# Kernel tuning notes

Hardware: AMD Instinct MI355X
Metric: run time of the kernel (lower is better)

## Reference

```python
import jax, jax.numpy as jnp
import numpy as np

E, P, T, B = 512, 128, 1024, 1


def _lstm_dir(x, wih, whh, bih, bhh, reverse):
    # x: [B, T, Din]; torch LSTM gate order: i, f, g, o
    Bb = x.shape[0]
    H = whh.shape[1]
    xg = jnp.einsum('btd,gd->btg', x, wih) + bih + bhh  # [B, T, 4H]
    xg = jnp.swapaxes(xg, 0, 1)  # [T, B, 4H]

    def step(carry, g_t):
        h, c = carry
        g = g_t + h @ whh.T
        i, f, gg, o = jnp.split(g, 4, axis=-1)
        c = jax.nn.sigmoid(f) * c + jax.nn.sigmoid(i) * jnp.tanh(gg)
        h = jax.nn.sigmoid(o) * jnp.tanh(c)
        return (h, c), h

    h0 = jnp.zeros((Bb, H), x.dtype)
    _, hs = jax.lax.scan(step, (h0, h0), xg, reverse=reverse)
    return jnp.swapaxes(hs, 0, 1)  # [B, T, H]


def _bilstm(x, layers):
    for wih, whh, bih, bhh in layers:
        f = _lstm_dir(x, wih[0], whh[0], bih[0], bhh[0], False)
        b = _lstm_dir(x, wih[1], whh[1], bih[1], bhh[1], True)
        x = jnp.concatenate([f, b], axis=-1)
    return x


def setup_inputs() -> dict:
    key = jax.random.key(0)
    ks = jax.random.split(key, 20)
    s = 0.05
    d = {
        'words': jax.random.normal(ks[0], (B, T, E), jnp.float32),
        'pos': jax.random.normal(ks[1], (B, T, P), jnp.float32),
        'w_w0_ih': s * jax.random.normal(ks[2], (2, 4 * E, E), jnp.float32),
        'w_w0_hh': s * jax.random.normal(ks[3], (2, 4 * E, E), jnp.float32),
        'w_b0_ih': s * jax.random.normal(ks[4], (2, 4 * E), jnp.float32),
        'w_b0_hh': s * jax.random.normal(ks[5], (2, 4 * E), jnp.float32),
        'w_w1_ih': s * jax.random.normal(ks[6], (2, 4 * E, 2 * E), jnp.float32),
        'w_w1_hh': s * jax.random.normal(ks[7], (2, 4 * E, E), jnp.float32),
        'w_b1_ih': s * jax.random.normal(ks[8], (2, 4 * E), jnp.float32),
        'w_b1_hh': s * jax.random.normal(ks[9], (2, 4 * E), jnp.float32),
        'p_w0_ih': s * jax.random.normal(ks[10], (2, 4 * P, P), jnp.float32),
        'p_w0_hh': s * jax.random.normal(ks[11], (2, 4 * P, P), jnp.float32),
        'p_b0_ih': s * jax.random.normal(ks[12], (2, 4 * P), jnp.float32),
        'p_b0_hh': s * jax.random.normal(ks[13], (2, 4 * P), jnp.float32),
        'p_w1_ih': s * jax.random.normal(ks[14], (2, 4 * P, 2 * P), jnp.float32),
        'p_w1_hh': s * jax.random.normal(ks[15], (2, 4 * P, P), jnp.float32),
        'p_b1_ih': s * jax.random.normal(ks[16], (2, 4 * P), jnp.float32),
        'p_b1_hh': s * jax.random.normal(ks[17], (2, 4 * P), jnp.float32),
        'edge_w': s * jax.random.normal(ks[18], (1, 4 * (E + P)), jnp.float32),
        'edge_b': s * jax.random.normal(ks[19], (1,), jnp.float32),
    }
    return d


def reference(words, pos, w_w0_ih, w_w0_hh, w_b0_ih, w_b0_hh, w_w1_ih, w_w1_hh,
              w_b1_ih, w_b1_hh, p_w0_ih, p_w0_hh, p_b0_ih, p_b0_hh, p_w1_ih,
              p_w1_hh, p_b1_ih, p_b1_hh, edge_w, edge_b):
    hw = _bilstm(words, [(w_w0_ih, w_w0_hh, w_b0_ih, w_b0_hh),
                         (w_w1_ih, w_w1_hh, w_b1_ih, w_b1_hh)])  # [B,T,2E]
    hp = _bilstm(pos, [(p_w0_ih, p_w0_hh, p_b0_ih, p_b0_hh),
                       (p_w1_ih, p_w1_hh, p_b1_ih, p_b1_hh)])    # [B,T,2P]
    H = jnp.concatenate([hw, hp], axis=-1)[0]  # [T, 2(E+P)]
    D = H.shape[-1]
    # edge_scorer(concat(h_i, h_j)) = h_i @ W1 + h_j @ W2 + b
    s1 = H @ edge_w[0, :D]  # [T]
    s2 = H @ edge_w[0, D:]  # [T]
    S = s1[:, None] + s2[None, :] + edge_b[0]
    n = H.shape[0]
    eye = jnp.eye(n, dtype=bool)
    return jnp.where(eye, jnp.zeros((), S.dtype), S)  # diagonal stays 0
```

## Files before the change

### kernel.cpp

```cpp
#include <hip/hip_runtime.h>


#define T_LEN 1024

__global__ void poison_kernel(unsigned* p, int n) {
  int i = blockIdx.x * blockDim.x + threadIdx.x;
  int stride = gridDim.x * blockDim.x;
  for (; i < n; i += stride) p[i] = 0xFFFFFFFFu;
}

__global__ __launch_bounds__(256) void gemm_bt(
    const float* __restrict__ A,
    const float* __restrict__ Wt,
    const float* __restrict__ B0,
    const float* __restrict__ B1,
    float* __restrict__ C,
    int M, int N, int K)
{
  const int z = blockIdx.z;
  const float* W  = Wt + (size_t)z * N * K;
  const float* b0 = B0 + (size_t)z * N;
  const float* b1 = B1 + (size_t)z * N;
  float* Cz = C + (size_t)z * M * N;

  __shared__ __align__(16) float As[16][64];
  __shared__ __align__(16) float Ws[16][64];

  const int tid = threadIdx.x;
  const int tx = tid & 15, ty = tid >> 4;
  const int brow = blockIdx.y * 64, bcol = blockIdx.x * 64;
  const int lr = tid >> 2;
  const int lk = (tid & 3) << 2;

  float acc[4][4] = {};

  for (int k0 = 0; k0 < K; k0 += 16) {
    float4 av = *(const float4*)(A + (size_t)(brow + lr) * K + k0 + lk);
    float4 wv = *(const float4*)(W + (size_t)(bcol + lr) * K + k0 + lk);
    __syncthreads();
    As[lk + 0][lr] = av.x; As[lk + 1][lr] = av.y;
    As[lk + 2][lr] = av.z; As[lk + 3][lr] = av.w;
    Ws[lk + 0][lr] = wv.x; Ws[lk + 1][lr] = wv.y;
    Ws[lk + 2][lr] = wv.z; Ws[lk + 3][lr] = wv.w;
    __syncthreads();
    #pragma unroll
    for (int kk = 0; kk < 16; ++kk) {
      float4 a = *(const float4*)&As[kk][ty << 2];
      float4 w = *(const float4*)&Ws[kk][tx << 2];
      float a4[4] = {a.x, a.y, a.z, a.w};
      float w4[4] = {w.x, w.y, w.z, w.w};
      #pragma unroll
      for (int i = 0; i < 4; ++i)
        #pragma unroll
        for (int j = 0; j < 4; ++j)
          acc[i][j] = fmaf(a4[i], w4[j], acc[i][j]);
    }
  }

  const int nb = bcol + (tx << 2);
  float bias[4];
  #pragma unroll
  for (int j = 0; j < 4; ++j) bias[j] = b0[nb + j] + b1[nb + j];
  #pragma unroll
  for (int i = 0; i < 4; ++i) {
    int m = brow + (ty << 2) + i;
    float4 out;
    out.x = acc[i][0] + bias[0];
    out.y = acc[i][1] + bias[1];
    out.z = acc[i][2] + bias[2];
    out.w = acc[i][3] + bias[3];
    *(float4*)(Cz + (size_t)m * N + nb) = out;
  }
}

__device__ __forceinline__ float fsigmoid(float x) {
  return 1.f / (1.f + __expf(-x));
}
__device__ __forceinline__ float ftanh(float x) {
  return 2.f / (1.f + __expf(-2.f * x)) - 1.f;
}

template<int CTRL>
__device__ __forceinline__ float dpp_add(float v) {
  int x = __builtin_amdgcn_update_dpp(0, __float_as_int(v), CTRL, 0xf, 0xf, true);
  return v + __int_as_float(x);
}

__device__ __forceinline__ void word_body(
    int wg, const float* __restrict__ xg, const float* __restrict__ whh,
    float* hbuf, int rev)
{
  const int tid  = threadIdx.x;
  const int wave = tid >> 6;
  const int lane = tid & 63;
  const int p    = lane & 31;
  const int half = lane >> 5;
  const int eloc = wave * 2 + half;
  const int e    = wg * 16 + eloc;

  float4 wv[4][4];
  #pragma unroll
  for (int g = 0; g < 4; ++g) {
    const float* row = whh + (size_t)(g * 512 + e) * 512 + 4 * p;
    #pragma unroll
    for (int k = 0; k < 4; ++k)
      wv[g][k] = *(const float4*)(row + 128 * k);
  }

  __shared__ __align__(16) float h_lds[512];
  __shared__ __align__(16) float4 hgates[16];

  unsigned* hb = (unsigned*)hbuf;
  unsigned long long* hb64 = (unsigned long long*)hbuf;

  const bool tail = (tid < 16);
  float cst = 0.f;
  float xg4[4] = {0.f, 0.f, 0.f, 0.f};
  if (tail) {
    const int t0 = rev ? (T_LEN - 1) : 0;
    #pragma unroll
    for (int g = 0; g < 4; ++g)
      xg4[g] = xg[(size_t)t0 * 2048 + g * 512 + wg * 16 + tid];
  }

  for (int s = 0; s < T_LEN; ++s) {
    const int t = rev ? (T_LEN - 1 - s) : s;

    if (tid < 256) {
      float2 v;
      if (s == 0) {
        v.x = 0.f; v.y = 0.f;
      } else {
        const int tp = rev ? (t + 1) : (t - 1);
        unsigned long long u = __hip_atomic_load(hb64 + (size_t)tp * 256 + tid,
                                                 __ATOMIC_RELAXED,
                                                 __HIP_MEMORY_SCOPE_AGENT);
        while ((unsigned)u == 0xFFFFFFFFu || (unsigned)(u >> 32) == 0xFFFFFFFFu)
          u = __hip_atomic_load(hb64 + (size_t)tp * 256 + tid,
                                __ATOMIC_RELAXED, __HIP_MEMORY_SCOPE_AGENT);
        v.x = __uint_as_float((unsigned)u);
        v.y = __uint_as_float((unsigned)(u >> 32));
      }
      *(float2*)&h_lds[2 * tid] = v;
    }
    __syncthreads();

    float a0 = 0.f, a1 = 0.f, a2 = 0.f, a3 = 0.f;
    #pragma unroll
    for (int k = 0; k < 4; ++k) {
      float4 hv = *(const float4*)&h_lds[128 * k + 4 * p];
      float h4[4] = {hv.x, hv.y, hv.z, hv.w};
      #pragma unroll
      for (int j = 0; j < 4; ++j) {
        a0 = fmaf(wv[0][k].x * 0.f + ((const float*)&wv[0][k])[j], h4[j], a0);
        a1 = fmaf(((const float*)&wv[1][k])[j], h4[j], a1);
        a2 = fmaf(((const float*)&wv[2][k])[j], h4[j], a2);
        a3 = fmaf(((const float*)&wv[3][k])[j], h4[j], a3);
      }
    }

    a0 = dpp_add<0xB1>(a0);  a1 = dpp_add<0xB1>(a1);
    a2 = dpp_add<0xB1>(a2);  a3 = dpp_add<0xB1>(a3);
    a0 = dpp_add<0x4E>(a0);  a1 = dpp_add<0x4E>(a1);
    a2 = dpp_add<0x4E>(a2);  a3 = dpp_add<0x4E>(a3);
    a0 = dpp_add<0x141>(a0); a1 = dpp_add<0x141>(a1);
    a2 = dpp_add<0x141>(a2); a3 = dpp_add<0x141>(a3);
    a0 = dpp_add<0x140>(a0); a1 = dpp_add<0x140>(a1);
    a2 = dpp_add<0x140>(a2); a3 = dpp_add<0x140>(a3);
    a0 = dpp_add<0x142>(a0); a1 = dpp_add<0x142>(a1);
    a2 = dpp_add<0x142>(a2); a3 = dpp_add<0x142>(a3);

    if (p == 16) {
      float4 gsum; gsum.x = a0; gsum.y = a1; gsum.z = a2; gsum.w = a3;
      hgates[eloc] = gsum;
    }
    __syncthreads();

    if (tail) {
      float4 g4 = hgates[tid];
      float si = fsigmoid(g4.x + xg4[0]);
      float sf = fsigmoid(g4.y + xg4[1]);
      float tg = ftanh  (g4.z + xg4[2]);
      float so = fsigmoid(g4.w + xg4[3]);
      cst = fmaf(sf, cst, si * tg);
      float h = so * ftanh(cst);
      __hip_atomic_store(hb + (size_t)t * 512 + wg * 16 + tid,
                         __float_as_uint(h),
                         __ATOMIC_RELAXED, __HIP_MEMORY_SCOPE_AGENT);
      if (s + 1 < T_LEN) {
        const int tn = rev ? (t - 1) : (t + 1);
        #pragma unroll
        for (int g = 0; g < 4; ++g)
          xg4[g] = xg[(size_t)tn * 2048 + g * 512 + wg * 16 + tid];
      }
    }
  }
}

__device__ __forceinline__ void pos_body(
    const float* __restrict__ xg, const float* __restrict__ whh,
    float* __restrict__ hbuf, int rev)
{
  const int tid = threadIdx.x;
  const int p   = tid & 3;
  const int e   = tid >> 2;

  float w[4][32];
  #pragma unroll
  for (int g = 0; g < 4; ++g) {
    const float* row = whh + (size_t)(g * 128 + e) * 128 + 4 * p;
    #pragma unroll
    for (int k = 0; k < 8; ++k) {
      float4 v = *(const float4*)(row + 16 * k);
      w[g][k * 4 + 0] = v.x; w[g][k * 4 + 1] = v.y;
      w[g][k * 4 + 2] = v.z; w[g][k * 4 + 3] = v.w;
    }
  }

  __shared__ __align__(16) float h_lds[2][128];

  float cst = 0.f;
  float xg4[4] = {0.f, 0.f, 0.f, 0.f};
  if (p == 0) {
    const int t0 = rev ? (T_LEN - 1) : 0;
    #pragma unroll
    for (int g = 0; g < 4; ++g) xg4[g] = xg[(size_t)t0 * 512 + g * 128 + e];
  }
  if (tid < 128) h_lds[0][tid] = 0.f;
  __syncthreads();

  for (int s = 0; s < T_LEN; ++s) {
    const int t   = rev ? (T_LEN - 1 - s) : s;
    const int buf = s & 1;

    float a0 = 0.f, a1 = 0.f, a2 = 0.f, a3 = 0.f;
    #pragma unroll
    for (int k = 0; k < 8; ++k) {
      float4 hv = *(const float4*)&h_lds[buf][16 * k + 4 * p];
      float h4[4] = {hv.x, hv.y, hv.z, hv.w};
      #pragma unroll
      for (int j = 0; j < 4; ++j) {
        a0 = fmaf(w[0][k * 4 + j], h4[j], a0);
        a1 = fmaf(w[1][k * 4 + j], h4[j], a1);
        a2 = fmaf(w[2][k * 4 + j], h4[j], a2);
        a3 = fmaf(w[3][k * 4 + j], h4[j], a3);
      }
    }
    a0 = dpp_add<0xB1>(a0); a1 = dpp_add<0xB1>(a1);
    a2 = dpp_add<0xB1>(a2); a3 = dpp_add<0xB1>(a3);
    a0 = dpp_add<0x4E>(a0); a1 = dpp_add<0x4E>(a1);
    a2 = dpp_add<0x4E>(a2); a3 = dpp_add<0x4E>(a3);

    if (p == 0) {
      float si = fsigmoid(a0 + xg4[0]);
      float sf = fsigmoid(a1 + xg4[1]);
      float tg = ftanh  (a2 + xg4[2]);
      float so = fsigmoid(a3 + xg4[3]);
      cst = fmaf(sf, cst, si * tg);
      float h = so * ftanh(cst);
      h_lds[buf ^ 1][e] = h;
      hbuf[(size_t)t * 128 + e] = h;
      if (s + 1 < T_LEN) {
        const int tn = rev ? (t - 1) : (t + 1);
        #pragma unroll
        for (int g = 0; g < 4; ++g)
          xg4[g] = xg[(size_t)tn * 512 + g * 128 + e];
      }
    }
    __syncthreads();
  }
}

__global__ __launch_bounds__(512, 1) void rec_kernel(
    const float* xg_wf, const float* xg_wb, const float* whh_w,
    float* h_wf, float* h_wb,
    const float* xg_pf, const float* xg_pb, const float* whh_p,
    float* h_pf, float* h_pb)
{
  int b = blockIdx.x;
  if (b < 32)
    word_body(b, xg_wf, whh_w, h_wf, 0);
  else if (b < 64)
    word_body(b - 32, xg_wb, whh_w + 2048 * 512, h_wb, 1);
  else if (b == 64)
    pos_body(xg_pf, whh_p, h_pf, 0);
  else
    pos_body(xg_pb, whh_p + 512 * 128, h_pb, 1);
}

__global__ void concat_k(const float* __restrict__ wf, const float* __restrict__ wb,
                         const float* __restrict__ pf, const float* __restrict__ pb,
                         float* __restrict__ wcat, float* __restrict__ pcat)
{
  const int totw = T_LEN * 1024;
  const int totp = T_LEN * 256;
  int idx = blockIdx.x * blockDim.x + threadIdx.x;
  int stride = gridDim.x * blockDim.x;
  for (int e = idx; e < totw + totp; e += stride) {
    if (e < totw) {
      int t = e >> 10, d = e & 1023;
      wcat[e] = d < 512 ? wf[t * 512 + d] : wb[t * 512 + (d - 512)];
    } else {
      int e2 = e - totw;
      int t = e2 >> 8, d = e2 & 255;
      pcat[e2] = d < 128 ? pf[t * 128 + d] : pb[t * 128 + (d - 128)];
    }
  }
}

__global__ __launch_bounds__(256) void edge_s(
    const float* __restrict__ hwf, const float* __restrict__ hwb,
    const float* __restrict__ hpf, const float* __restrict__ hpb,
    const float* __restrict__ ew, float* s1, float* s2)
{
  const int i = blockIdx.x;
  const int tid = threadIdx.x;
  float a1 = 0.f, a2 = 0.f;
  for (int d = tid; d < 1280; d += 256) {
    float hv;
    if (d < 512)       hv = hwf[i * 512 + d];
    else if (d < 1024) hv = hwb[i * 512 + d - 512];
    else if (d < 1152) hv = hpf[i * 128 + d - 1024];
    else               hv = hpb[i * 128 + d - 1152];
    a1 = fmaf(hv, ew[d], a1);
    a2 = fmaf(hv, ew[1280 + d], a2);
  }
  #pragma unroll
  for (int off = 32; off > 0; off >>= 1) {
    a1 += __shfl_xor(a1, off, 64);
    a2 += __shfl_xor(a2, off, 64);
  }
  __shared__ float r1[4], r2[4];
  const int wid = tid >> 6;
  if ((tid & 63) == 0) { r1[wid] = a1; r2[wid] = a2; }
  __syncthreads();
  if (tid == 0) {
    s1[i] = (r1[0] + r1[1]) + (r1[2] + r1[3]);
    s2[i] = (r2[0] + r2[1]) + (r2[2] + r2[3]);
  }
}

__global__ __launch_bounds__(256) void sfill(
    const float* __restrict__ s1, const float* __restrict__ s2,
    const float* __restrict__ eb, float* __restrict__ out)
{
  int e = blockIdx.x * 256 + threadIdx.x;
  int i = e >> 10, j = e & 1023;
  out[e] = (i == j) ? 0.f : s1[i] + s2[j] + eb[0];
}

extern "C" void kernel_launch(void* const* d_in, const int* in_sizes, int n_in,
                              void* d_out, int out_size, void* d_ws, size_t ws_size,
                              hipStream_t stream)
{
  const float* words   = (const float*)d_in[0];
  const float* pos     = (const float*)d_in[1];
  const float* w_w0_ih = (const float*)d_in[2];
  const float* w_w0_hh = (const float*)d_in[3];
  const float* w_b0_ih = (const float*)d_in[4];
  const float* w_b0_hh = (const float*)d_in[5];
  const float* w_w1_ih = (const float*)d_in[6];
  const float* w_w1_hh = (const float*)d_in[7];
  const float* w_b1_ih = (const float*)d_in[8];
  const float* w_b1_hh = (const float*)d_in[9];
  const float* p_w0_ih = (const float*)d_in[10];
  const float* p_w0_hh = (const float*)d_in[11];
  const float* p_b0_ih = (const float*)d_in[12];
  const float* p_b0_hh = (const float*)d_in[13];
  const float* p_w1_ih = (const float*)d_in[14];
  const float* p_w1_hh = (const float*)d_in[15];
  const float* p_b1_ih = (const float*)d_in[16];
  const float* p_b1_hh = (const float*)d_in[17];
  const float* edge_w  = (const float*)d_in[18];
  const float* edge_b  = (const float*)d_in[19];

  float* ws = (float*)d_ws;
  float* xg_w  = ws;
  float* xg_p  = ws + 4194304;
  float* hw0_f = ws + 5242880;
  float* hw0_b = hw0_f + 524288;
  float* hw1_f = hw0_b + 524288;
  float* hw1_b = hw1_f + 524288;
  float* hp0_f = hw1_b + 524288;
  float* hp0_b = hp0_f + 131072;
  float* hp1_f = hp0_b + 131072;
  float* hp1_b = hp1_f + 131072;
  float* wcat  = hp1_b + 131072;
  float* pcat  = wcat + 1048576;
  float* s1    = pcat + 262144;
  float* s2    = s1 + 1024;

  poison_kernel<<<1024, 256, 0, stream>>>((unsigned*)hw0_f, 2097152);

  gemm_bt<<<dim3(32, 16, 2), 256, 0, stream>>>(words, w_w0_ih, w_b0_ih, w_b0_hh,
                                               xg_w, 1024, 2048, 512);
  gemm_bt<<<dim3(8, 16, 2), 256, 0, stream>>>(pos, p_w0_ih, p_b0_ih, p_b0_hh,
                                              xg_p, 1024, 512, 128);

  rec_kernel<<<66, 512, 0, stream>>>(xg_w, xg_w + 2097152, w_w0_hh, hw0_f, hw0_b,
                                     xg_p, xg_p + 524288, p_w0_hh, hp0_f, hp0_b);

  concat_k<<<2048, 256, 0, stream>>>(hw0_f, hw0_b, hp0_f, hp0_b, wcat, pcat);

  gemm_bt<<<dim3(32, 16, 2), 256, 0, stream>>>(wcat, w_w1_ih, w_b1_ih, w_b1_hh,
                                               xg_w, 1024, 2048, 1024);
  gemm_bt<<<dim3(8, 16, 2), 256, 0, stream>>>(pcat, p_w1_ih, p_b1_ih, p_b1_hh,
                                              xg_p, 1024, 512, 256);

  rec_kernel<<<66, 512, 0, stream>>>(xg_w, xg_w + 2097152, w_w1_hh, hw1_f, hw1_b,
                                     xg_p, xg_p + 524288, p_w1_hh, hp1_f, hp1_b);

  edge_s<<<1024, 256, 0, stream>>>(hw1_f, hw1_b, hp1_f, hp1_b, edge_w, s1, s2);
  sfill<<<4096, 256, 0, stream>>>(s1, s2, edge_b, (float*)d_out);
}
```

Before: 3.343 ms.

## Double-buffer hidden state and replace a barrier with LDS flag handoff in word LSTM

The word-LSTM recurrent kernel now double-buffers the hidden state in LDS, and waves 1-4 poll for the next step's global h while the current step's gates are reduced. The barrier between the gate reduction and the tail cell update is replaced by sentinel-flagged volatile LDS slots that the tail threads spin on, leaving one barrier per step instead of two. This aims to cut per-step latency on the serial recurrence. It relies on implicit ordering of LDS writes across waves without fences, which is fragile, and it also drops a dead multiply-by-zero.

```diff
diff --git a/kernel.cpp b/kernel.cpp
--- a/kernel.cpp
+++ b/kernel.cpp
@@ -107,13 +107,14 @@
       wv[g][k] = *(const float4*)(row + 128 * k);
   }
 
-  __shared__ __align__(16) float h_lds[512];
-  __shared__ __align__(16) float4 hgates[16];
+  __shared__ __align__(16) float h_lds[2][512];
+  __shared__ __align__(16) unsigned hgates4[16][4];
 
   unsigned* hb = (unsigned*)hbuf;
   unsigned long long* hb64 = (unsigned long long*)hbuf;
 
-  const bool tail = (tid < 16);
+  const bool tail   = (tid < 16);
+  const bool poller = (tid >= 64 && tid < 320);
   float cst = 0.f;
   float xg4[4] = {0.f, 0.f, 0.f, 0.f};
   if (tail) {
@@ -123,36 +124,25 @@
       xg4[g] = xg[(size_t)t0 * 2048 + g * 512 + wg * 16 + tid];
   }
 
+  h_lds[0][tid] = 0.f;
+  if (tid < 16) {
+    hgates4[tid][0] = 0xFFFFFFFFu; hgates4[tid][1] = 0xFFFFFFFFu;
+    hgates4[tid][2] = 0xFFFFFFFFu; hgates4[tid][3] = 0xFFFFFFFFu;
+  }
+  __syncthreads();
+
   for (int s = 0; s < T_LEN; ++s) {
-    const int t = rev ? (T_LEN - 1 - s) : s;
-
-    if (tid < 256) {
-      float2 v;
-      if (s == 0) {
-        v.x = 0.f; v.y = 0.f;
-      } else {
-        const int tp = rev ? (t + 1) : (t - 1);
-        unsigned long long u = __hip_atomic_load(hb64 + (size_t)tp * 256 + tid,
-                                                 __ATOMIC_RELAXED,
-                                                 __HIP_MEMORY_SCOPE_AGENT);
-        while ((unsigned)u == 0xFFFFFFFFu || (unsigned)(u >> 32) == 0xFFFFFFFFu)
-          u = __hip_atomic_load(hb64 + (size_t)tp * 256 + tid,
-                                __ATOMIC_RELAXED, __HIP_MEMORY_SCOPE_AGENT);
-        v.x = __uint_as_float((unsigned)u);
-        v.y = __uint_as_float((unsigned)(u >> 32));
-      }
-      *(float2*)&h_lds[2 * tid] = v;
-    }
-    __syncthreads();
+    const int t   = rev ? (T_LEN - 1 - s) : s;
+    const int buf = s & 1;
 
     float a0 = 0.f, a1 = 0.f, a2 = 0.f, a3 = 0.f;
     #pragma unroll
     for (int k = 0; k < 4; ++k) {
-      float4 hv = *(const float4*)&h_lds[128 * k + 4 * p];
+      float4 hv = *(const float4*)&h_lds[buf][128 * k + 4 * p];
       float h4[4] = {hv.x, hv.y, hv.z, hv.w};
       #pragma unroll
       for (int j = 0; j < 4; ++j) {
-        a0 = fmaf(wv[0][k].x * 0.f + ((const float*)&wv[0][k])[j], h4[j], a0);
+        a0 = fmaf(((const float*)&wv[0][k])[j], h4[j], a0);
         a1 = fmaf(((const float*)&wv[1][k])[j], h4[j], a1);
         a2 = fmaf(((const float*)&wv[2][k])[j], h4[j], a2);
         a3 = fmaf(((const float*)&wv[3][k])[j], h4[j], a3);
@@ -171,17 +161,39 @@
     a2 = dpp_add<0x142>(a2); a3 = dpp_add<0x142>(a3);
 
     if (p == 16) {
-      float4 gsum; gsum.x = a0; gsum.y = a1; gsum.z = a2; gsum.w = a3;
-      hgates[eloc] = gsum;
-    }
-    __syncthreads();
+      volatile unsigned* hg = &hgates4[eloc][0];
+      hg[0] = __float_as_uint(a0);
+      hg[1] = __float_as_uint(a1);
+      hg[2] = __float_as_uint(a2);
+      hg[3] = __float_as_uint(a3);
+    }
+    asm volatile("" ::: "memory");
+
+    if (poller && s + 1 < T_LEN) {
+      const int g = tid - 64;
+      unsigned long long u = __hip_atomic_load(hb64 + (size_t)t * 256 + g,
+                                               __ATOMIC_RELAXED,
+                                               __HIP_MEMORY_SCOPE_AGENT);
+      while ((unsigned)u == 0xFFFFFFFFu || (unsigned)(u >> 32) == 0xFFFFFFFFu)
+        u = __hip_atomic_load(hb64 + (size_t)t * 256 + g,
+                              __ATOMIC_RELAXED, __HIP_MEMORY_SCOPE_AGENT);
+      h_lds[buf ^ 1][2 * g]     = __uint_as_float((unsigned)u);
+      h_lds[buf ^ 1][2 * g + 1] = __uint_as_float((unsigned)(u >> 32));
+    }
 
     if (tail) {
-      float4 g4 = hgates[tid];
-      float si = fsigmoid(g4.x + xg4[0]);
-      float sf = fsigmoid(g4.y + xg4[1]);
-      float tg = ftanh  (g4.z + xg4[2]);
-      float so = fsigmoid(g4.w + xg4[3]);
+      volatile unsigned* hg = &hgates4[tid][0];
+      unsigned x0, x1, x2, x3;
+      do {
+        x0 = hg[0]; x1 = hg[1]; x2 = hg[2]; x3 = hg[3];
+      } while (x0 == 0xFFFFFFFFu || x1 == 0xFFFFFFFFu ||
+               x2 == 0xFFFFFFFFu || x3 == 0xFFFFFFFFu);
+      hg[0] = 0xFFFFFFFFu; hg[1] = 0xFFFFFFFFu;
+      hg[2] = 0xFFFFFFFFu; hg[3] = 0xFFFFFFFFu;
+      float si = fsigmoid(__uint_as_float(x0) + xg4[0]);
+      float sf = fsigmoid(__uint_as_float(x1) + xg4[1]);
+      float tg = ftanh  (__uint_as_float(x2) + xg4[2]);
+      float so = fsigmoid(__uint_as_float(x3) + xg4[3]);
       cst = fmaf(sf, cst, si * tg);
       float h = so * ftanh(cst);
       __hip_atomic_store(hb + (size_t)t * 512 + wg * 16 + tid,
@@ -194,6 +206,8 @@
           xg4[g] = xg[(size_t)tn * 2048 + g * 512 + wg * 16 + tid];
       }
     }
+
+    __syncthreads();
   }
 }
 
```

Result: slower. 3.634 ms (+8.7%).
